# Optimization experiments

Measured on AMD Instinct MI355X. Metric: run time of the kernel, lower is better.

Reference implementation:

```python
import jax, jax.numpy as jnp
import numpy as np

B, N, C, T, M, H, W = 4, 500, 80, 28, 16, 800, 800
ALPHA, GAMMA, EPS = 0.25, 2.0, 1e-8
CAND_K = 10          # SimOTA candidate top-k
CTR_R = 0.25         # center-radius fraction for in-center test
CLS_W, L1_W, GIOU_W, MASK_W = 2.0, 5.0, 2.0, 5.0
IMG = 800.0


def _rand_boxes(key, shape, lo, hi):
    k1, k2 = jax.random.split(key)
    ctr = jax.random.uniform(k1, shape + (2,), minval=hi / 2, maxval=IMG - hi / 2)
    wh = jax.random.uniform(k2, shape + (2,), minval=lo, maxval=hi)
    return jnp.concatenate([ctr - wh / 2, ctr + wh / 2], axis=-1)


def setup_inputs() -> dict:
    key = jax.random.key(0)
    ks = jax.random.split(key, 6)
    return {
        'pred_logits': jax.random.normal(ks[0], (B, N, C), jnp.float32),
        'pred_boxes': _rand_boxes(ks[1], (B, N), 40.0, 320.0),
        'pred_masks': jax.random.normal(ks[2], (B, N, C, T, T), jnp.float32),
        'gt_classes': jax.random.randint(ks[3], (B, M), 0, C),
        'gt_boxes': _rand_boxes(ks[4], (B, M), 60.0, 400.0),
        'gt_masks': (jax.random.uniform(ks[5], (B, M, H, W)) > 0.5).astype(jnp.float32),
        'image_size': jnp.full((B, 4), IMG, jnp.float32),
    }


def _box_iou_union(b1, b2):
    lt = jnp.maximum(b1[..., :2], b2[..., :2])
    rb = jnp.minimum(b1[..., 2:], b2[..., 2:])
    wh = jnp.clip(rb - lt, 0.0)
    inter = wh[..., 0] * wh[..., 1]
    a1 = (b1[..., 2] - b1[..., 0]) * (b1[..., 3] - b1[..., 1])
    a2 = (b2[..., 2] - b2[..., 0]) * (b2[..., 3] - b2[..., 1])
    union = a1 + a2 - inter
    return inter / (union + EPS), union


def _giou(b1, b2):
    iou, union = _box_iou_union(b1, b2)
    lt = jnp.minimum(b1[..., :2], b2[..., :2])
    rb = jnp.maximum(b1[..., 2:], b2[..., 2:])
    wh = jnp.clip(rb - lt, 0.0)
    enc = wh[..., 0] * wh[..., 1]
    return iou - (enc - union) / (enc + EPS)


def _crop_resize(mask, box):
    # ROIAlign-style bilinear crop of a [H,W] bitmask to [T,T], then binarize (detectron2 semantics)
    x1, y1, x2, y2 = box[0], box[1], box[2], box[3]
    xs = x1 + (jnp.arange(T) + 0.5) * (x2 - x1) / T - 0.5
    ys = y1 + (jnp.arange(T) + 0.5) * (y2 - y1) / T - 0.5
    yy, xx = jnp.meshgrid(ys, xs, indexing='ij')
    s = jax.scipy.ndimage.map_coordinates(mask, [yy, xx], order=1, mode='constant')
    return (s >= 0.5).astype(jnp.float32)


def _per_image(logits, boxes, masks, gt_cls, gt_boxes, gt_masks_flat, image_size):
    # logits [N,C], boxes [N,4] xyxy, masks [N,C,T,T], gt_cls [M], gt_boxes [M,4], gt_masks_flat [M,T*T]
    cx = (boxes[:, 0] + boxes[:, 2]) * 0.5
    cy = (boxes[:, 1] + boxes[:, 3]) * 0.5
    in_box = ((cx[:, None] > gt_boxes[None, :, 0]) & (cx[:, None] < gt_boxes[None, :, 2]) &
              (cy[:, None] > gt_boxes[None, :, 1]) & (cy[:, None] < gt_boxes[None, :, 3]))
    gcx = (gt_boxes[:, 0] + gt_boxes[:, 2]) * 0.5
    gcy = (gt_boxes[:, 1] + gt_boxes[:, 3]) * 0.5
    gw = gt_boxes[:, 2] - gt_boxes[:, 0]
    gh = gt_boxes[:, 3] - gt_boxes[:, 1]
    in_ctr = ((jnp.abs(cx[:, None] - gcx[None, :]) < CTR_R * gw[None, :]) &
              (jnp.abs(cy[:, None] - gcy[None, :]) < CTR_R * gh[None, :]))
    valid = (in_box | in_ctr).any(axis=1)          # [N]
    in_both = in_box & in_ctr                       # [N,M]

    p = jax.nn.sigmoid(logits)
    neg = -jnp.log(1.0 - p + EPS) * (1.0 - ALPHA) * p ** GAMMA
    pos = -jnp.log(p + EPS) * ALPHA * (1.0 - p) ** GAMMA
    cls_cost = CLS_W * (pos - neg)[:, gt_cls]       # [N,M]

    nb = boxes / image_size
    ngb = gt_boxes / image_size
    l1_cost = L1_W * jnp.abs(nb[:, None, :] - ngb[None, :, :]).sum(-1)
    giou_cost = GIOU_W * (1.0 - _giou(nb[:, None, :], ngb[None, :, :]))

    ms = jax.nn.sigmoid(masks).reshape(N, C, T * T)
    inter = jnp.einsum('nct,mt->nmc', ms, gt_masks_flat)
    union = ms.sum(-1)[:, None, :] + gt_masks_flat.sum(-1)[None, :, None] + EPS
    dice = 1.0 - 2.0 * inter / union                # [N,M,C]
    mask_cost = MASK_W * dice[:, jnp.arange(M), gt_cls]

    cost = (cls_cost + l1_cost + giou_cost + mask_cost
            + (~in_both).astype(jnp.float32) * 1e5
            + (~valid)[:, None].astype(jnp.float32) * 1e9)
    cost = jax.lax.stop_gradient(cost)              # matcher is @no_grad

    ious, _ = _box_iou_union(boxes[:, None, :], gt_boxes[None, :, :])
    ious = jax.lax.stop_gradient(ious * valid[:, None].astype(jnp.float32))
    topk_ious, _ = jax.lax.top_k(ious.T, CAND_K)    # [M,K]
    dyn_k = jnp.clip(topk_ious.sum(-1).astype(jnp.int32), 1, None)

    def col_match(cost_col, dk):
        _, idx = jax.lax.top_k(-cost_col, CAND_K)
        sel = (jnp.arange(CAND_K) < dk).astype(jnp.float32)
        return jnp.zeros((N,), jnp.float32).at[idx].add(sel)

    matching = jax.vmap(col_match, in_axes=(1, 0), out_axes=1)(cost, dyn_k)  # [N,M]
    multi = matching.sum(axis=1) > 1
    best = jnp.argmin(cost, axis=1)
    matching = jnp.where(multi[:, None], jax.nn.one_hot(best, M, dtype=jnp.float32), matching)
    fg = (matching.sum(axis=1) > 0) & valid
    wgt = fg.astype(jnp.float32)                    # [N]
    matched = jnp.argmax(matching, axis=1)          # [N]

    tcls = gt_cls[matched]
    tgt = jax.nn.one_hot(tcls, C, dtype=jnp.float32)
    ce = jnp.maximum(logits, 0.0) - logits * tgt + jnp.log1p(jnp.exp(-jnp.abs(logits)))
    pt = p * tgt + (1.0 - p) * (1.0 - tgt)
    focal = ce * (1.0 - pt) ** GAMMA * (ALPHA * tgt + (1.0 - ALPHA) * (1.0 - tgt))
    cls_loss = (focal.sum(-1) * wgt).sum()

    mgb = ngb[matched]
    l1_loss = (jnp.abs(nb - mgb).sum(-1) * wgt).sum()
    giou_loss = ((1.0 - _giou(nb, mgb)) * wgt).sum()

    pm = ms[jnp.arange(N), tcls]                    # [N,T*T]
    gm = gt_masks_flat[matched]
    mi = (pm * gm).sum(-1)
    mu = pm.sum(-1) + gm.sum(-1) + EPS
    mask_loss = ((1.0 - 2.0 * mi / mu) * wgt).sum()
    return cls_loss, l1_loss, giou_loss, mask_loss, wgt.sum()


def reference(pred_logits, pred_boxes, pred_masks, gt_classes, gt_boxes, gt_masks, image_size):
    gm_flat = jax.vmap(jax.vmap(_crop_resize))(gt_masks, gt_boxes).reshape(B, M, T * T)
    cl, l1, gi, mk, ni = jax.vmap(_per_image)(
        pred_logits, pred_boxes, pred_masks, gt_classes, gt_boxes, gm_flat, image_size)
    n = ni.sum()
    return jnp.stack([CLS_W * cl.sum() / n, L1_W * l1.sum() / n,
                      GIOU_W * gi.sum() / n, MASK_W * mk.sum() / n])
```

## Files before the change

kernel.cpp:

```cpp
#include <hip/hip_runtime.h>
#include <math.h>

#define B_ 4
#define N_ 500
#define C_ 80
#define T_ 28
#define TT 784
#define M_ 16
#define H_ 800
#define W_ 800
#define CAND_K 10
#define EPS 1e-8f

#define OFF_GM    0
#define OFF_GSUM  (OFF_GM + B_*M_*TT)
#define OFF_COST  (OFF_GSUM + B_*M_)
#define OFF_IOUS  (OFF_COST + B_*N_*M_)
#define OFF_MATCH (OFF_IOUS + B_*N_*M_)
#define OFF_VALID (OFF_MATCH + B_*N_*M_)
#define OFF_ACC   (OFF_VALID + B_*N_)
#define WS_FLOATS (OFF_ACC + 8)

__global__ __launch_bounds__(256) void crop_kernel(
    const float* __restrict__ gtm, const float* __restrict__ gboxes,
    float* __restrict__ gm, float* __restrict__ gsum, float* __restrict__ acc) {
  if (blockIdx.x == 0 && threadIdx.x < 8) acc[threadIdx.x] = 0.f;
  int bm = blockIdx.x;
  const float* img = gtm + (size_t)bm * (H_ * W_);
  float x1 = gboxes[bm*4+0], y1 = gboxes[bm*4+1];
  float x2 = gboxes[bm*4+2], y2 = gboxes[bm*4+3];
  float part = 0.f;
  for (int t = threadIdx.x; t < TT; t += blockDim.x) {
    int i = t / T_, j = t - i * T_;
    float y = y1 + (i + 0.5f) * (y2 - y1) / T_ - 0.5f;
    float x = x1 + (j + 0.5f) * (x2 - x1) / T_ - 0.5f;
    int y0 = (int)floorf(y), x0 = (int)floorf(x);
    float fy = y - (float)y0, fx = x - (float)x0;
    float v = 0.f;
#pragma unroll
    for (int dy = 0; dy < 2; ++dy)
#pragma unroll
      for (int dx = 0; dx < 2; ++dx) {
        int yy = y0 + dy, xx = x0 + dx;
        float w = (dy ? fy : 1.f - fy) * (dx ? fx : 1.f - fx);
        if (yy >= 0 && yy < H_ && xx >= 0 && xx < W_)
          v += w * img[yy * W_ + xx];
      }
    float g = (v >= 0.5f) ? 1.f : 0.f;
    gm[(size_t)bm * TT + t] = g;
    part += g;
  }
  __shared__ float sb[4];
  for (int off = 32; off; off >>= 1) part += __shfl_down(part, off, 64);
  int lane = threadIdx.x & 63, w = threadIdx.x >> 6;
  if (lane == 0) sb[w] = part;
  __syncthreads();
  if (threadIdx.x == 0) gsum[bm] = sb[0] + sb[1] + sb[2] + sb[3];
}

__global__ __launch_bounds__(256) void cost_kernel(
    const float* __restrict__ logits, const float* __restrict__ boxes,
    const float* __restrict__ masks, const int* __restrict__ gcls,
    const float* __restrict__ gboxes, const float* __restrict__ imgsz,
    const float* __restrict__ gm, const float* __restrict__ gsum,
    float* __restrict__ cost, float* __restrict__ ious,
    float* __restrict__ validf) {
  int blk = blockIdx.x;
  int b = blk / N_, n = blk - b * N_;
  int tid = threadIdx.x;
  int lane = tid & 63, wave = tid >> 6;
  __shared__ float s_ssum[M_], s_inter[M_];
  const size_t nb_off = (size_t)(b * N_ + n);

  for (int m = wave; m < M_; m += 4) {
    int gc = gcls[b * M_ + m];
    const float4* mp = (const float4*)(masks + (nb_off * C_ + gc) * TT);
    const float4* gp = (const float4*)(gm + (size_t)(b * M_ + m) * TT);
    float si = 0.f, sg = 0.f;
    for (int t = lane; t < TT / 4; t += 64) {
      float4 mv = mp[t];
      float4 gv = gp[t];
      float p0 = 1.f / (1.f + expf(-mv.x));
      float p1 = 1.f / (1.f + expf(-mv.y));
      float p2 = 1.f / (1.f + expf(-mv.z));
      float p3 = 1.f / (1.f + expf(-mv.w));
      si += p0 + p1 + p2 + p3;
      sg += p0 * gv.x + p1 * gv.y + p2 * gv.z + p3 * gv.w;
    }
    for (int off = 32; off; off >>= 1) {
      si += __shfl_down(si, off, 64);
      sg += __shfl_down(sg, off, 64);
    }
    if (lane == 0) { s_ssum[m] = si; s_inter[m] = sg; }
  }
  __syncthreads();

  float bx1 = boxes[nb_off*4+0], by1 = boxes[nb_off*4+1];
  float bx2 = boxes[nb_off*4+2], by2 = boxes[nb_off*4+3];
  float cx = (bx1 + bx2) * 0.5f, cy = (by1 + by2) * 0.5f;
  bool flag = false, in_box = false, in_ctr = false;
  float gx1 = 0, gy1 = 0, gx2 = 0, gy2 = 0;
  if (tid < M_) {
    int gi = (b * M_ + tid) * 4;
    gx1 = gboxes[gi+0]; gy1 = gboxes[gi+1]; gx2 = gboxes[gi+2]; gy2 = gboxes[gi+3];
    in_box = (cx > gx1) && (cx < gx2) && (cy > gy1) && (cy < gy2);
    float gcx = (gx1 + gx2) * 0.5f, gcy = (gy1 + gy2) * 0.5f;
    float gw = gx2 - gx1, gh = gy2 - gy1;
    in_ctr = (fabsf(cx - gcx) < 0.25f * gw) && (fabsf(cy - gcy) < 0.25f * gh);
    flag = in_box || in_ctr;
  }
  unsigned long long bal = __ballot(flag);
  bool valid = (bal != 0ULL);
  if (tid == 0) validf[nb_off] = valid ? 1.f : 0.f;

  if (tid < M_) {
    int m = tid;
    int gc = gcls[b * M_ + m];
    float lg = logits[nb_off * C_ + gc];
    float p = 1.f / (1.f + expf(-lg));
    float pos = -logf(p + EPS) * 0.25f * (1.f - p) * (1.f - p);
    float neg = -logf(1.f - p + EPS) * 0.75f * p * p;
    float ccost = 2.f * (pos - neg);
    float s0 = imgsz[b*4+0], s1 = imgsz[b*4+1], s2 = imgsz[b*4+2], s3 = imgsz[b*4+3];
    float nbx1 = bx1/s0, nby1 = by1/s1, nbx2 = bx2/s2, nby2 = by2/s3;
    float ngx1 = gx1/s0, ngy1 = gy1/s1, ngx2 = gx2/s2, ngy2 = gy2/s3;
    float l1 = 5.f * (fabsf(nbx1-ngx1) + fabsf(nby1-ngy1) +
                      fabsf(nbx2-ngx2) + fabsf(nby2-ngy2));
    float ilx = fmaxf(nbx1, ngx1), ily = fmaxf(nby1, ngy1);
    float irx = fminf(nbx2, ngx2), iry = fminf(nby2, ngy2);
    float iw = fmaxf(irx - ilx, 0.f), ih = fmaxf(iry - ily, 0.f);
    float inter = iw * ih;
    float a1 = (nbx2 - nbx1) * (nby2 - nby1);
    float a2 = (ngx2 - ngx1) * (ngy2 - ngy1);
    float uni = a1 + a2 - inter;
    float iou = inter / (uni + EPS);
    float elx = fminf(nbx1, ngx1), ely = fminf(nby1, ngy1);
    float erx = fmaxf(nbx2, ngx2), ery = fmaxf(nby2, ngy2);
    float ew = fmaxf(erx - elx, 0.f), eh = fmaxf(ery - ely, 0.f);
    float enc = ew * eh;
    float giou = iou - (enc - uni) / (enc + EPS);
    float gcost = 2.f * (1.f - giou);
    float mcost = 5.f * (1.f - 2.f * s_inter[m] / (s_ssum[m] + gsum[b*M_+m] + EPS));
    float c = ccost + l1 + gcost + mcost;
    if (!(in_box && in_ctr)) c += 1e5f;
    if (!valid) c += 1e9f;
    cost[nb_off * M_ + m] = c;
    float rlx = fmaxf(bx1, gx1), rly = fmaxf(by1, gy1);
    float rrx = fminf(bx2, gx2), rry = fminf(by2, gy2);
    float rw = fmaxf(rrx - rlx, 0.f), rh = fmaxf(rry - rly, 0.f);
    float rinter = rw * rh;
    float ra1 = (bx2 - bx1) * (by2 - by1);
    float ra2 = (gx2 - gx1) * (gy2 - gy1);
    float runi = ra1 + ra2 - rinter;
    float riou = rinter / (runi + EPS);
    ious[nb_off * M_ + m] = valid ? riou : 0.f;
  }
}

__global__ __launch_bounds__(256) void match_kernel(
    const float* __restrict__ cost, const float* __restrict__ ious,
    float* __restrict__ matching) {
  int b = blockIdx.x / M_, m = blockIdx.x - b * M_;
  int tid = threadIdx.x;
  __shared__ float cc[N_], io[N_];
  __shared__ float swv[4];
  __shared__ int swi[4];
  __shared__ int s_dk;
  for (int n = tid; n < N_; n += 256) {
    cc[n] = cost[(size_t)(b * N_ + n) * M_ + m];
    io[n] = ious[(size_t)(b * N_ + n) * M_ + m];
    matching[(size_t)(b * N_ + n) * M_ + m] = 0.f;
  }
  __syncthreads();
  int lane = tid & 63, w = tid >> 6;
  float s = 0.f;
  for (int k = 0; k < CAND_K; ++k) {
    float bv = -1e30f; int bi = 0x7fffffff;
    for (int n = tid; n < N_; n += 256) {
      float v = io[n];
      if (v > bv || (v == bv && n < bi)) { bv = v; bi = n; }
    }
    for (int off = 32; off; off >>= 1) {
      float ov = __shfl_down(bv, off, 64);
      int oi = __shfl_down(bi, off, 64);
      if (ov > bv || (ov == bv && oi < bi)) { bv = ov; bi = oi; }
    }
    if (lane == 0) { swv[w] = bv; swi[w] = bi; }
    __syncthreads();
    if (tid == 0) {
      float Bv = swv[0]; int Bi = swi[0];
      for (int ww = 1; ww < 4; ++ww)
        if (swv[ww] > Bv || (swv[ww] == Bv && swi[ww] < Bi)) { Bv = swv[ww]; Bi = swi[ww]; }
      s += Bv;
      io[Bi] = -1e30f;
    }
    __syncthreads();
  }
  if (tid == 0) {
    int dk = (int)s;
    if (dk < 1) dk = 1;
    s_dk = dk;
  }
  __syncthreads();
  int dk = s_dk;
  for (int k = 0; k < CAND_K; ++k) {
    float bv = 1e30f; int bi = 0x7fffffff;
    for (int n = tid; n < N_; n += 256) {
      float v = cc[n];
      if (v < bv || (v == bv && n < bi)) { bv = v; bi = n; }
    }
    for (int off = 32; off; off >>= 1) {
      float ov = __shfl_down(bv, off, 64);
      int oi = __shfl_down(bi, off, 64);
      if (ov < bv || (ov == bv && oi < bi)) { bv = ov; bi = oi; }
    }
    if (lane == 0) { swv[w] = bv; swi[w] = bi; }
    __syncthreads();
    if (tid == 0) {
      float Bv = swv[0]; int Bi = swi[0];
      for (int ww = 1; ww < 4; ++ww)
        if (swv[ww] < Bv || (swv[ww] == Bv && swi[ww] < Bi)) { Bv = swv[ww]; Bi = swi[ww]; }
      if (k < dk) matching[(size_t)(b * N_ + Bi) * M_ + m] = 1.f;
      cc[Bi] = 1e30f;
    }
    __syncthreads();
  }
}

__global__ __launch_bounds__(256) void loss_kernel(
    const float* __restrict__ logits, const float* __restrict__ boxes,
    const float* __restrict__ masks, const int* __restrict__ gcls,
    const float* __restrict__ gboxes, const float* __restrict__ imgsz,
    const float* __restrict__ gm, const float* __restrict__ gsum,
    const float* __restrict__ matching, const float* __restrict__ cost,
    const float* __restrict__ validf, float* __restrict__ acc) {
  int gid = blockIdx.x * blockDim.x + threadIdx.x;
  int wid = gid >> 6;
  int lane = threadIdx.x & 63;
  if (wid >= B_ * N_) return;
  int b = wid / N_, n = wid - b * N_;
  size_t nb_off = (size_t)(b * N_ + n);

  int matched = 0, fg = 0;
  if (lane == 0) {
    const float* mrow = matching + nb_off * M_;
    const float* crow = cost + nb_off * M_;
    float msum = 0.f; int first = -1;
    for (int m = 0; m < M_; ++m) {
      float v = mrow[m];
      msum += v;
      if (first < 0 && v > 0.5f) first = m;
    }
    float fgs;
    if (msum > 1.f) {
      float bv = crow[0]; int bi = 0;
      for (int m = 1; m < M_; ++m) if (crow[m] < bv) { bv = crow[m]; bi = m; }
      matched = bi; fgs = 1.f;
    } else {
      matched = (first >= 0) ? first : 0;
      fgs = msum;
    }
    fg = (fgs > 0.f && validf[nb_off] > 0.5f) ? 1 : 0;
  }
  matched = __shfl(matched, 0, 64);
  fg = __shfl(fg, 0, 64);
  if (!fg) return;

  int tcls = gcls[b * M_ + matched];
  float fsum = 0.f;
  for (int c = lane; c < C_; c += 64) {
    float l = logits[nb_off * C_ + c];
    float p = 1.f / (1.f + expf(-l));
    float tgt = (c == tcls) ? 1.f : 0.f;
    float ce = fmaxf(l, 0.f) - l * tgt + log1pf(expf(-fabsf(l)));
    float pt = p * tgt + (1.f - p) * (1.f - tgt);
    float om = 1.f - pt;
    float wf = 0.25f * tgt + 0.75f * (1.f - tgt);
    fsum += ce * om * om * wf;
  }
  float mi = 0.f, ps = 0.f;
  const float* pmrow = masks + (nb_off * C_ + tcls) * TT;
  const float* gmrow = gm + (size_t)(b * M_ + matched) * TT;
  for (int t = lane; t < TT; t += 64) {
    float pm = 1.f / (1.f + expf(-pmrow[t]));
    mi += pm * gmrow[t];
    ps += pm;
  }
  for (int off = 32; off; off >>= 1) {
    fsum += __shfl_down(fsum, off, 64);
    mi   += __shfl_down(mi, off, 64);
    ps   += __shfl_down(ps, off, 64);
  }
  if (lane == 0) {
    float bx1 = boxes[nb_off*4+0], by1 = boxes[nb_off*4+1];
    float bx2 = boxes[nb_off*4+2], by2 = boxes[nb_off*4+3];
    int gi = (b * M_ + matched) * 4;
    float gx1 = gboxes[gi+0], gy1 = gboxes[gi+1], gx2 = gboxes[gi+2], gy2 = gboxes[gi+3];
    float s0 = imgsz[b*4+0], s1 = imgsz[b*4+1], s2 = imgsz[b*4+2], s3 = imgsz[b*4+3];
    float nbx1 = bx1/s0, nby1 = by1/s1, nbx2 = bx2/s2, nby2 = by2/s3;
    float ngx1 = gx1/s0, ngy1 = gy1/s1, ngx2 = gx2/s2, ngy2 = gy2/s3;
    float l1 = fabsf(nbx1-ngx1) + fabsf(nby1-ngy1) + fabsf(nbx2-ngx2) + fabsf(nby2-ngy2);
    float ilx = fmaxf(nbx1, ngx1), ily = fmaxf(nby1, ngy1);
    float irx = fminf(nbx2, ngx2), iry = fminf(nby2, ngy2);
    float iw = fmaxf(irx - ilx, 0.f), ih = fmaxf(iry - ily, 0.f);
    float inter = iw * ih;
    float a1 = (nbx2 - nbx1) * (nby2 - nby1);
    float a2 = (ngx2 - ngx1) * (ngy2 - ngy1);
    float uni = a1 + a2 - inter;
    float iou = inter / (uni + EPS);
    float elx = fminf(nbx1, ngx1), ely = fminf(nby1, ngy1);
    float erx = fmaxf(nbx2, ngx2), ery = fmaxf(nby2, ngy2);
    float ew = fmaxf(erx - elx, 0.f), eh = fmaxf(ery - ely, 0.f);
    float enc = ew * eh;
    float giou = iou - (enc - uni) / (enc + EPS);
    float gterm = 1.f - giou;
    float mu = ps + gsum[b * M_ + matched] + EPS;
    float mterm = 1.f - 2.f * mi / mu;
    atomicAdd(&acc[0], fsum);
    atomicAdd(&acc[1], l1);
    atomicAdd(&acc[2], gterm);
    atomicAdd(&acc[3], mterm);
    atomicAdd(&acc[4], 1.f);
  }
}

__global__ void finalize_kernel(const float* __restrict__ acc, float* __restrict__ out) {
  if (threadIdx.x == 0 && blockIdx.x == 0) {
    float nf = acc[4];
    out[0] = 2.f * acc[0] / nf;
    out[1] = 5.f * acc[1] / nf;
    out[2] = 2.f * acc[2] / nf;
    out[3] = 5.f * acc[3] / nf;
  }
}

extern "C" void kernel_launch(void* const* d_in, const int* in_sizes, int n_in,
                              void* d_out, int out_size, void* d_ws, size_t ws_size,
                              hipStream_t stream) {
  const float* logits = (const float*)d_in[0];
  const float* boxes  = (const float*)d_in[1];
  const float* masks  = (const float*)d_in[2];
  const int*   gcls   = (const int*)d_in[3];
  const float* gboxes = (const float*)d_in[4];
  const float* gtm    = (const float*)d_in[5];
  const float* imgsz  = (const float*)d_in[6];

  float* ws       = (float*)d_ws;
  float* gm       = ws + OFF_GM;
  float* gsum     = ws + OFF_GSUM;
  float* cost     = ws + OFF_COST;
  float* ious     = ws + OFF_IOUS;
  float* matching = ws + OFF_MATCH;
  float* validf   = ws + OFF_VALID;
  float* acc      = ws + OFF_ACC;

  crop_kernel<<<B_ * M_, 256, 0, stream>>>(gtm, gboxes, gm, gsum, acc);
  cost_kernel<<<B_ * N_, 256, 0, stream>>>(logits, boxes, masks, gcls, gboxes,
                                           imgsz, gm, gsum, cost, ious, validf);
  match_kernel<<<B_ * M_, 256, 0, stream>>>(cost, ious, matching);
  loss_kernel<<<(B_ * N_ * 64 + 255) / 256, 256, 0, stream>>>(
      logits, boxes, masks, gcls, gboxes, imgsz, gm, gsum, matching, cost,
      validf, acc);
  finalize_kernel<<<1, 64, 0, stream>>>(acc, (float*)d_out);
}
```

Baseline: 685.1 us.

## Skip mask cost for invalid preds, cache mask sums, single-wave matching, fuse finalize

The cost kernel now checks validity first and computes the sigmoid mask sums only for valid predictions. It stores the per-(n,m) mask intersection and sum into the workspace so the loss kernel reads them instead of re-reading and re-sigmoiding mask rows. The matching kernel becomes a single 64-lane wave that keeps candidates in registers, removing shared-memory barriers. The finalize kernel is folded into the loss kernel through a last-block atomic counter, and the crop loop is unrolled. Together these cut memory traffic and launch overhead. In exchange the code adds extra workspace arrays and depends on a counter that must be reset on every run.

```diff
diff --git a/kernel.cpp b/kernel.cpp
--- a/kernel.cpp
+++ b/kernel.cpp
@@ -17,9 +17,10 @@
 #define OFF_COST  (OFF_GSUM + B_*M_)
 #define OFF_IOUS  (OFF_COST + B_*N_*M_)
 #define OFF_MATCH (OFF_IOUS + B_*N_*M_)
-#define OFF_VALID (OFF_MATCH + B_*N_*M_)
+#define OFF_SSUM  (OFF_MATCH + B_*N_*M_)
+#define OFF_INTER (OFF_SSUM + B_*N_*M_)
+#define OFF_VALID (OFF_INTER + B_*N_*M_)
 #define OFF_ACC   (OFF_VALID + B_*N_)
-#define WS_FLOATS (OFF_ACC + 8)
 
 __global__ __launch_bounds__(256) void crop_kernel(
     const float* __restrict__ gtm, const float* __restrict__ gboxes,
@@ -30,8 +31,12 @@
   float x1 = gboxes[bm*4+0], y1 = gboxes[bm*4+1];
   float x2 = gboxes[bm*4+2], y2 = gboxes[bm*4+3];
   float part = 0.f;
-  for (int t = threadIdx.x; t < TT; t += blockDim.x) {
-    int i = t / T_, j = t - i * T_;
+#pragma unroll
+  for (int r = 0; r < 4; ++r) {
+    int t = threadIdx.x + r * 256;
+    bool on = t < TT;
+    int tc = on ? t : 0;
+    int i = tc / T_, j = tc - i * T_;
     float y = y1 + (i + 0.5f) * (y2 - y1) / T_ - 0.5f;
     float x = x1 + (j + 0.5f) * (x2 - x1) / T_ - 0.5f;
     int y0 = (int)floorf(y), x0 = (int)floorf(x);
@@ -43,12 +48,14 @@
       for (int dx = 0; dx < 2; ++dx) {
         int yy = y0 + dy, xx = x0 + dx;
         float w = (dy ? fy : 1.f - fy) * (dx ? fx : 1.f - fx);
-        if (yy >= 0 && yy < H_ && xx >= 0 && xx < W_)
+        if (on && yy >= 0 && yy < H_ && xx >= 0 && xx < W_)
           v += w * img[yy * W_ + xx];
       }
-    float g = (v >= 0.5f) ? 1.f : 0.f;
-    gm[(size_t)bm * TT + t] = g;
-    part += g;
+    if (on) {
+      float g = (v >= 0.5f) ? 1.f : 0.f;
+      gm[(size_t)bm * TT + t] = g;
+      part += g;
+    }
   }
   __shared__ float sb[4];
   for (int off = 32; off; off >>= 1) part += __shfl_down(part, off, 64);
@@ -64,7 +71,8 @@
     const float* __restrict__ gboxes, const float* __restrict__ imgsz,
     const float* __restrict__ gm, const float* __restrict__ gsum,
     float* __restrict__ cost, float* __restrict__ ious,
-    float* __restrict__ validf) {
+    float* __restrict__ validf, float* __restrict__ ssumb,
+    float* __restrict__ interb) {
   int blk = blockIdx.x;
   int b = blk / N_, n = blk - b * N_;
   int tid = threadIdx.x;
@@ -72,36 +80,13 @@
   __shared__ float s_ssum[M_], s_inter[M_];
   const size_t nb_off = (size_t)(b * N_ + n);
 
-  for (int m = wave; m < M_; m += 4) {
-    int gc = gcls[b * M_ + m];
-    const float4* mp = (const float4*)(masks + (nb_off * C_ + gc) * TT);
-    const float4* gp = (const float4*)(gm + (size_t)(b * M_ + m) * TT);
-    float si = 0.f, sg = 0.f;
-    for (int t = lane; t < TT / 4; t += 64) {
-      float4 mv = mp[t];
-      float4 gv = gp[t];
-      float p0 = 1.f / (1.f + expf(-mv.x));
-      float p1 = 1.f / (1.f + expf(-mv.y));
-      float p2 = 1.f / (1.f + expf(-mv.z));
-      float p3 = 1.f / (1.f + expf(-mv.w));
-      si += p0 + p1 + p2 + p3;
-      sg += p0 * gv.x + p1 * gv.y + p2 * gv.z + p3 * gv.w;
-    }
-    for (int off = 32; off; off >>= 1) {
-      si += __shfl_down(si, off, 64);
-      sg += __shfl_down(sg, off, 64);
-    }
-    if (lane == 0) { s_ssum[m] = si; s_inter[m] = sg; }
-  }
-  __syncthreads();
-
   float bx1 = boxes[nb_off*4+0], by1 = boxes[nb_off*4+1];
   float bx2 = boxes[nb_off*4+2], by2 = boxes[nb_off*4+3];
   float cx = (bx1 + bx2) * 0.5f, cy = (by1 + by2) * 0.5f;
   bool flag = false, in_box = false, in_ctr = false;
   float gx1 = 0, gy1 = 0, gx2 = 0, gy2 = 0;
-  if (tid < M_) {
-    int gi = (b * M_ + tid) * 4;
+  if (lane < M_) {
+    int gi = (b * M_ + lane) * 4;
     gx1 = gboxes[gi+0]; gy1 = gboxes[gi+1]; gx2 = gboxes[gi+2]; gy2 = gboxes[gi+3];
     in_box = (cx > gx1) && (cx < gx2) && (cy > gy1) && (cy < gy2);
     float gcx = (gx1 + gx2) * 0.5f, gcy = (gy1 + gy2) * 0.5f;
@@ -109,8 +94,51 @@
     in_ctr = (fabsf(cx - gcx) < 0.25f * gw) && (fabsf(cy - gcy) < 0.25f * gh);
     flag = in_box || in_ctr;
   }
-  unsigned long long bal = __ballot(flag);
-  bool valid = (bal != 0ULL);
+  bool valid = (__ballot(flag) != 0ULL);
+
+  if (valid) {
+    const float* mbase = masks + nb_off * C_ * TT;
+    const float* gbase = gm + (size_t)b * M_ * TT;
+#pragma unroll
+    for (int mm = 0; mm < 4; ++mm) {
+      int m = wave + mm * 4;
+      int gc = gcls[b * M_ + m];
+      const float4* mp = (const float4*)(mbase + (size_t)gc * TT);
+      const float4* gp = (const float4*)(gbase + (size_t)m * TT);
+      float4 a0 = mp[lane], a1 = mp[lane + 64], a2 = mp[lane + 128];
+      float4 g0 = gp[lane], g1 = gp[lane + 64], g2 = gp[lane + 128];
+      float4 a3 = make_float4(0,0,0,0), g3 = make_float4(0,0,0,0);
+      if (lane < 4) { a3 = mp[192 + lane]; g3 = gp[192 + lane]; }
+      float si = 0.f, sg = 0.f;
+      {
+        float p0 = 1.f/(1.f+expf(-a0.x)), p1 = 1.f/(1.f+expf(-a0.y));
+        float p2 = 1.f/(1.f+expf(-a0.z)), p3 = 1.f/(1.f+expf(-a0.w));
+        si += p0+p1+p2+p3; sg += p0*g0.x+p1*g0.y+p2*g0.z+p3*g0.w;
+      }
+      {
+        float p0 = 1.f/(1.f+expf(-a1.x)), p1 = 1.f/(1.f+expf(-a1.y));
+        float p2 = 1.f/(1.f+expf(-a1.z)), p3 = 1.f/(1.f+expf(-a1.w));
+        si += p0+p1+p2+p3; sg += p0*g1.x+p1*g1.y+p2*g1.z+p3*g1.w;
+      }
+      {
+        float p0 = 1.f/(1.f+expf(-a2.x)), p1 = 1.f/(1.f+expf(-a2.y));
+        float p2 = 1.f/(1.f+expf(-a2.z)), p3 = 1.f/(1.f+expf(-a2.w));
+        si += p0+p1+p2+p3; sg += p0*g2.x+p1*g2.y+p2*g2.z+p3*g2.w;
+      }
+      if (lane < 4) {
+        float p0 = 1.f/(1.f+expf(-a3.x)), p1 = 1.f/(1.f+expf(-a3.y));
+        float p2 = 1.f/(1.f+expf(-a3.z)), p3 = 1.f/(1.f+expf(-a3.w));
+        si += p0+p1+p2+p3; sg += p0*g3.x+p1*g3.y+p2*g3.z+p3*g3.w;
+      }
+      for (int off = 32; off; off >>= 1) {
+        si += __shfl_down(si, off, 64);
+        sg += __shfl_down(sg, off, 64);
+      }
+      if (lane == 0) { s_ssum[m] = si; s_inter[m] = sg; }
+    }
+  }
+  __syncthreads();
+
   if (tid == 0) validf[nb_off] = valid ? 1.f : 0.f;
 
   if (tid < M_) {
@@ -140,11 +168,17 @@
     float enc = ew * eh;
     float giou = iou - (enc - uni) / (enc + EPS);
     float gcost = 2.f * (1.f - giou);
-    float mcost = 5.f * (1.f - 2.f * s_inter[m] / (s_ssum[m] + gsum[b*M_+m] + EPS));
+    float mcost = valid
+        ? 5.f * (1.f - 2.f * s_inter[m] / (s_ssum[m] + gsum[b*M_+m] + EPS))
+        : 0.f;
     float c = ccost + l1 + gcost + mcost;
     if (!(in_box && in_ctr)) c += 1e5f;
     if (!valid) c += 1e9f;
     cost[nb_off * M_ + m] = c;
+    if (valid) {
+      ssumb[nb_off * M_ + m] = s_ssum[m];
+      interb[nb_off * M_ + m] = s_inter[m];
+    }
     float rlx = fmaxf(bx1, gx1), rly = fmaxf(by1, gy1);
     float rrx = fminf(bx2, gx2), rry = fminf(by2, gy2);
     float rw = fmaxf(rrx - rlx, 0.f), rh = fmaxf(rry - rly, 0.f);
@@ -157,180 +191,175 @@
   }
 }
 
-__global__ __launch_bounds__(256) void match_kernel(
+__global__ __launch_bounds__(64) void match_kernel(
     const float* __restrict__ cost, const float* __restrict__ ious,
     float* __restrict__ matching) {
   int b = blockIdx.x / M_, m = blockIdx.x - b * M_;
-  int tid = threadIdx.x;
-  __shared__ float cc[N_], io[N_];
-  __shared__ float swv[4];
-  __shared__ int swi[4];
-  __shared__ int s_dk;
-  for (int n = tid; n < N_; n += 256) {
-    cc[n] = cost[(size_t)(b * N_ + n) * M_ + m];
-    io[n] = ious[(size_t)(b * N_ + n) * M_ + m];
-    matching[(size_t)(b * N_ + n) * M_ + m] = 0.f;
-  }
-  __syncthreads();
-  int lane = tid & 63, w = tid >> 6;
+  int lane = threadIdx.x;
+  int base = b * N_;
+  float io[8], cc[8], msel[8];
+#pragma unroll
+  for (int r = 0; r < 8; ++r) {
+    int n = lane + 64 * r;
+    msel[r] = 0.f;
+    if (n < N_) {
+      io[r] = ious[(size_t)(base + n) * M_ + m];
+      cc[r] = cost[(size_t)(base + n) * M_ + m];
+    } else { io[r] = -1e30f; cc[r] = 1e30f; }
+  }
   float s = 0.f;
   for (int k = 0; k < CAND_K; ++k) {
     float bv = -1e30f; int bi = 0x7fffffff;
-    for (int n = tid; n < N_; n += 256) {
-      float v = io[n];
-      if (v > bv || (v == bv && n < bi)) { bv = v; bi = n; }
+#pragma unroll
+    for (int r = 0; r < 8; ++r) {
+      int n = lane + 64 * r;
+      if (io[r] > bv) { bv = io[r]; bi = n; }
     }
     for (int off = 32; off; off >>= 1) {
       float ov = __shfl_down(bv, off, 64);
       int oi = __shfl_down(bi, off, 64);
       if (ov > bv || (ov == bv && oi < bi)) { bv = ov; bi = oi; }
     }
-    if (lane == 0) { swv[w] = bv; swi[w] = bi; }
-    __syncthreads();
-    if (tid == 0) {
-      float Bv = swv[0]; int Bi = swi[0];
-      for (int ww = 1; ww < 4; ++ww)
-        if (swv[ww] > Bv || (swv[ww] == Bv && swi[ww] < Bi)) { Bv = swv[ww]; Bi = swi[ww]; }
-      s += Bv;
-      io[Bi] = -1e30f;
-    }
-    __syncthreads();
-  }
-  if (tid == 0) {
-    int dk = (int)s;
-    if (dk < 1) dk = 1;
-    s_dk = dk;
-  }
-  __syncthreads();
-  int dk = s_dk;
+    bv = __shfl(bv, 0, 64); bi = __shfl(bi, 0, 64);
+    s += bv;
+    int rsel = bi >> 6;
+#pragma unroll
+    for (int r = 0; r < 8; ++r)
+      if (r == rsel && (bi & 63) == lane) io[r] = -1e30f;
+  }
+  int dk = (int)s;
+  if (dk < 1) dk = 1;
   for (int k = 0; k < CAND_K; ++k) {
     float bv = 1e30f; int bi = 0x7fffffff;
-    for (int n = tid; n < N_; n += 256) {
-      float v = cc[n];
-      if (v < bv || (v == bv && n < bi)) { bv = v; bi = n; }
+#pragma unroll
+    for (int r = 0; r < 8; ++r) {
+      int n = lane + 64 * r;
+      if (cc[r] < bv) { bv = cc[r]; bi = n; }
     }
     for (int off = 32; off; off >>= 1) {
       float ov = __shfl_down(bv, off, 64);
       int oi = __shfl_down(bi, off, 64);
       if (ov < bv || (ov == bv && oi < bi)) { bv = ov; bi = oi; }
     }
-    if (lane == 0) { swv[w] = bv; swi[w] = bi; }
-    __syncthreads();
-    if (tid == 0) {
-      float Bv = swv[0]; int Bi = swi[0];
-      for (int ww = 1; ww < 4; ++ww)
-        if (swv[ww] < Bv || (swv[ww] == Bv && swi[ww] < Bi)) { Bv = swv[ww]; Bi = swi[ww]; }
-      if (k < dk) matching[(size_t)(b * N_ + Bi) * M_ + m] = 1.f;
-      cc[Bi] = 1e30f;
-    }
-    __syncthreads();
+    bi = __shfl(bi, 0, 64);
+    int rsel = bi >> 6;
+#pragma unroll
+    for (int r = 0; r < 8; ++r)
+      if (r == rsel && (bi & 63) == lane) {
+        cc[r] = 1e30f;
+        if (k < dk) msel[r] = 1.f;
+      }
+  }
+#pragma unroll
+  for (int r = 0; r < 8; ++r) {
+    int n = lane + 64 * r;
+    if (n < N_) matching[(size_t)(base + n) * M_ + m] = msel[r];
   }
 }
 
 __global__ __launch_bounds__(256) void loss_kernel(
     const float* __restrict__ logits, const float* __restrict__ boxes,
-    const float* __restrict__ masks, const int* __restrict__ gcls,
-    const float* __restrict__ gboxes, const float* __restrict__ imgsz,
-    const float* __restrict__ gm, const float* __restrict__ gsum,
+    const int* __restrict__ gcls, const float* __restrict__ gboxes,
+    const float* __restrict__ imgsz, const float* __restrict__ gsum,
     const float* __restrict__ matching, const float* __restrict__ cost,
-    const float* __restrict__ validf, float* __restrict__ acc) {
-  int gid = blockIdx.x * blockDim.x + threadIdx.x;
-  int wid = gid >> 6;
+    const float* __restrict__ validf, const float* __restrict__ ssumb,
+    const float* __restrict__ interb, float* __restrict__ acc,
+    float* __restrict__ out) {
+  int wid = blockIdx.x * 4 + (threadIdx.x >> 6);
   int lane = threadIdx.x & 63;
-  if (wid >= B_ * N_) return;
-  int b = wid / N_, n = wid - b * N_;
-  size_t nb_off = (size_t)(b * N_ + n);
-
-  int matched = 0, fg = 0;
-  if (lane == 0) {
-    const float* mrow = matching + nb_off * M_;
-    const float* crow = cost + nb_off * M_;
-    float msum = 0.f; int first = -1;
-    for (int m = 0; m < M_; ++m) {
-      float v = mrow[m];
-      msum += v;
-      if (first < 0 && v > 0.5f) first = m;
-    }
-    float fgs;
-    if (msum > 1.f) {
-      float bv = crow[0]; int bi = 0;
-      for (int m = 1; m < M_; ++m) if (crow[m] < bv) { bv = crow[m]; bi = m; }
-      matched = bi; fgs = 1.f;
-    } else {
-      matched = (first >= 0) ? first : 0;
-      fgs = msum;
-    }
-    fg = (fgs > 0.f && validf[nb_off] > 0.5f) ? 1 : 0;
-  }
-  matched = __shfl(matched, 0, 64);
-  fg = __shfl(fg, 0, 64);
-  if (!fg) return;
-
-  int tcls = gcls[b * M_ + matched];
-  float fsum = 0.f;
-  for (int c = lane; c < C_; c += 64) {
-    float l = logits[nb_off * C_ + c];
-    float p = 1.f / (1.f + expf(-l));
-    float tgt = (c == tcls) ? 1.f : 0.f;
-    float ce = fmaxf(l, 0.f) - l * tgt + log1pf(expf(-fabsf(l)));
-    float pt = p * tgt + (1.f - p) * (1.f - tgt);
-    float om = 1.f - pt;
-    float wf = 0.25f * tgt + 0.75f * (1.f - tgt);
-    fsum += ce * om * om * wf;
-  }
-  float mi = 0.f, ps = 0.f;
-  const float* pmrow = masks + (nb_off * C_ + tcls) * TT;
-  const float* gmrow = gm + (size_t)(b * M_ + matched) * TT;
-  for (int t = lane; t < TT; t += 64) {
-    float pm = 1.f / (1.f + expf(-pmrow[t]));
-    mi += pm * gmrow[t];
-    ps += pm;
-  }
-  for (int off = 32; off; off >>= 1) {
-    fsum += __shfl_down(fsum, off, 64);
-    mi   += __shfl_down(mi, off, 64);
-    ps   += __shfl_down(ps, off, 64);
-  }
-  if (lane == 0) {
-    float bx1 = boxes[nb_off*4+0], by1 = boxes[nb_off*4+1];
-    float bx2 = boxes[nb_off*4+2], by2 = boxes[nb_off*4+3];
-    int gi = (b * M_ + matched) * 4;
-    float gx1 = gboxes[gi+0], gy1 = gboxes[gi+1], gx2 = gboxes[gi+2], gy2 = gboxes[gi+3];
-    float s0 = imgsz[b*4+0], s1 = imgsz[b*4+1], s2 = imgsz[b*4+2], s3 = imgsz[b*4+3];
-    float nbx1 = bx1/s0, nby1 = by1/s1, nbx2 = bx2/s2, nby2 = by2/s3;
-    float ngx1 = gx1/s0, ngy1 = gy1/s1, ngx2 = gx2/s2, ngy2 = gy2/s3;
-    float l1 = fabsf(nbx1-ngx1) + fabsf(nby1-ngy1) + fabsf(nbx2-ngx2) + fabsf(nby2-ngy2);
-    float ilx = fmaxf(nbx1, ngx1), ily = fmaxf(nby1, ngy1);
-    float irx = fminf(nbx2, ngx2), iry = fminf(nby2, ngy2);
-    float iw = fmaxf(irx - ilx, 0.f), ih = fmaxf(iry - ily, 0.f);
-    float inter = iw * ih;
-    float a1 = (nbx2 - nbx1) * (nby2 - nby1);
-    float a2 = (ngx2 - ngx1) * (ngy2 - ngy1);
-    float uni = a1 + a2 - inter;
-    float iou = inter / (uni + EPS);
-    float elx = fminf(nbx1, ngx1), ely = fminf(nby1, ngy1);
-    float erx = fmaxf(nbx2, ngx2), ery = fmaxf(nby2, ngy2);
-    float ew = fmaxf(erx - elx, 0.f), eh = fmaxf(ery - ely, 0.f);
-    float enc = ew * eh;
-    float giou = iou - (enc - uni) / (enc + EPS);
-    float gterm = 1.f - giou;
-    float mu = ps + gsum[b * M_ + matched] + EPS;
-    float mterm = 1.f - 2.f * mi / mu;
-    atomicAdd(&acc[0], fsum);
-    atomicAdd(&acc[1], l1);
-    atomicAdd(&acc[2], gterm);
-    atomicAdd(&acc[3], mterm);
-    atomicAdd(&acc[4], 1.f);
-  }
-}
-
-__global__ void finalize_kernel(const float* __restrict__ acc, float* __restrict__ out) {
-  if (threadIdx.x == 0 && blockIdx.x == 0) {
-    float nf = acc[4];
-    out[0] = 2.f * acc[0] / nf;
-    out[1] = 5.f * acc[1] / nf;
-    out[2] = 2.f * acc[2] / nf;
-    out[3] = 5.f * acc[3] / nf;
+  {
+    int b = wid / N_, n = wid - b * N_;
+    size_t nb_off = (size_t)(b * N_ + n);
+    int matched = 0, fg = 0;
+    if (lane == 0) {
+      const float* mrow = matching + nb_off * M_;
+      const float* crow = cost + nb_off * M_;
+      float msum = 0.f; int first = -1;
+      for (int m = 0; m < M_; ++m) {
+        float v = mrow[m];
+        msum += v;
+        if (first < 0 && v > 0.5f) first = m;
+      }
+      float fgs;
+      if (msum > 1.f) {
+        float bv = crow[0]; int bi = 0;
+        for (int m = 1; m < M_; ++m) if (crow[m] < bv) { bv = crow[m]; bi = m; }
+        matched = bi; fgs = 1.f;
+      } else {
+        matched = (first >= 0) ? first : 0;
+        fgs = msum;
+      }
+      fg = (fgs > 0.f && validf[nb_off] > 0.5f) ? 1 : 0;
+    }
+    matched = __shfl(matched, 0, 64);
+    fg = __shfl(fg, 0, 64);
+    if (fg) {
+      int tcls = gcls[b * M_ + matched];
+      float fsum = 0.f;
+#pragma unroll
+      for (int rr = 0; rr < 2; ++rr) {
+        int c = lane + 64 * rr;
+        if (c < C_) {
+          float l = logits[nb_off * C_ + c];
+          float p = 1.f / (1.f + expf(-l));
+          float tgt = (c == tcls) ? 1.f : 0.f;
+          float ce = fmaxf(l, 0.f) - l * tgt + log1pf(expf(-fabsf(l)));
+          float pt = p * tgt + (1.f - p) * (1.f - tgt);
+          float om = 1.f - pt;
+          float wf = 0.25f * tgt + 0.75f * (1.f - tgt);
+          fsum += ce * om * om * wf;
+        }
+      }
+      for (int off = 32; off; off >>= 1) fsum += __shfl_down(fsum, off, 64);
+      if (lane == 0) {
+        float bx1 = boxes[nb_off*4+0], by1 = boxes[nb_off*4+1];
+        float bx2 = boxes[nb_off*4+2], by2 = boxes[nb_off*4+3];
+        int gi = (b * M_ + matched) * 4;
+        float gx1 = gboxes[gi+0], gy1 = gboxes[gi+1];
+        float gx2 = gboxes[gi+2], gy2 = gboxes[gi+3];
+        float s0 = imgsz[b*4+0], s1 = imgsz[b*4+1], s2 = imgsz[b*4+2], s3 = imgsz[b*4+3];
+        float nbx1 = bx1/s0, nby1 = by1/s1, nbx2 = bx2/s2, nby2 = by2/s3;
+        float ngx1 = gx1/s0, ngy1 = gy1/s1, ngx2 = gx2/s2, ngy2 = gy2/s3;
+        float l1 = fabsf(nbx1-ngx1) + fabsf(nby1-ngy1) + fabsf(nbx2-ngx2) + fabsf(nby2-ngy2);
+        float ilx = fmaxf(nbx1, ngx1), ily = fmaxf(nby1, ngy1);
+        float irx = fminf(nbx2, ngx2), iry = fminf(nby2, ngy2);
+        float iw = fmaxf(irx - ilx, 0.f), ih = fmaxf(iry - ily, 0.f);
+        float inter = iw * ih;
+        float a1 = (nbx2 - nbx1) * (nby2 - nby1);
+        float a2 = (ngx2 - ngx1) * (ngy2 - ngy1);
+        float uni = a1 + a2 - inter;
+        float iou = inter / (uni + EPS);
+        float elx = fminf(nbx1, ngx1), ely = fminf(nby1, ngy1);
+        float erx = fmaxf(nbx2, ngx2), ery = fmaxf(nby2, ngy2);
+        float ew = fmaxf(erx - elx, 0.f), eh = fmaxf(ery - ely, 0.f);
+        float enc = ew * eh;
+        float giou = iou - (enc - uni) / (enc + EPS);
+        float mi = interb[nb_off * M_ + matched];
+        float ps = ssumb[nb_off * M_ + matched];
+        float mu = ps + gsum[b * M_ + matched] + EPS;
+        atomicAdd(&acc[0], fsum);
+        atomicAdd(&acc[1], l1);
+        atomicAdd(&acc[2], 1.f - giou);
+        atomicAdd(&acc[3], 1.f - 2.f * mi / mu);
+        atomicAdd(&acc[4], 1.f);
+      }
+    }
+  }
+  __syncthreads();
+  if (threadIdx.x == 0) {
+    __threadfence();
+    int old = atomicAdd((int*)&acc[6], 1);
+    if (old == (int)gridDim.x - 1) {
+      float a0 = atomicAdd(&acc[0], 0.f);
+      float a1 = atomicAdd(&acc[1], 0.f);
+      float a2 = atomicAdd(&acc[2], 0.f);
+      float a3 = atomicAdd(&acc[3], 0.f);
+      float nf = atomicAdd(&acc[4], 0.f);
+      out[0] = 2.f * a0 / nf;
+      out[1] = 5.f * a1 / nf;
+      out[2] = 2.f * a2 / nf;
+      out[3] = 5.f * a3 / nf;
+    }
   }
 }
 
@@ -351,15 +380,17 @@
   float* cost     = ws + OFF_COST;
   float* ious     = ws + OFF_IOUS;
   float* matching = ws + OFF_MATCH;
+  float* ssumb    = ws + OFF_SSUM;
+  float* interb   = ws + OFF_INTER;
   float* validf   = ws + OFF_VALID;
   float* acc      = ws + OFF_ACC;
 
   crop_kernel<<<B_ * M_, 256, 0, stream>>>(gtm, gboxes, gm, gsum, acc);
   cost_kernel<<<B_ * N_, 256, 0, stream>>>(logits, boxes, masks, gcls, gboxes,
-                                           imgsz, gm, gsum, cost, ious, validf);
-  match_kernel<<<B_ * M_, 256, 0, stream>>>(cost, ious, matching);
-  loss_kernel<<<(B_ * N_ * 64 + 255) / 256, 256, 0, stream>>>(
-      logits, boxes, masks, gcls, gboxes, imgsz, gm, gsum, matching, cost,
-      validf, acc);
-  finalize_kernel<<<1, 64, 0, stream>>>(acc, (float*)d_out);
-}
+                                           imgsz, gm, gsum, cost, ious, validf,
+                                           ssumb, interb);
+  match_kernel<<<B_ * M_, 64, 0, stream>>>(cost, ious, matching);
+  loss_kernel<<<B_ * N_ / 4, 256, 0, stream>>>(
+      logits, boxes, gcls, gboxes, imgsz, gsum, matching, cost, validf,
+      ssumb, interb, acc, (float*)d_out);
+}
```

Result: no change. 680.1 us (-0.7%).
